# Performance work log

Measured on AMD Instinct MI355X. Metric: run time of the kernel, lower is better.

## Reference

```python
import jax, jax.numpy as jnp
import numpy as np

N_NODES = 100000
N_EDGES = 320000
DIM = 256


def _graph_conv(src, dst, h, W, b):
    # DGL GraphConv, norm='both', in_feats == out_feats (aggregate-then-transform)
    ones = jnp.ones((src.shape[0],), dtype=h.dtype)
    out_deg = jnp.clip(jax.ops.segment_sum(ones, src, num_segments=N_NODES), 1.0)
    in_deg = jnp.clip(jax.ops.segment_sum(ones, dst, num_segments=N_NODES), 1.0)
    h = h * (out_deg ** -0.5)[:, None]          # src-side normalization
    agg = jax.ops.segment_sum(h[src], dst, num_segments=N_NODES)  # SpMM (copy_u, sum)
    agg = agg * (in_deg ** -0.5)[:, None]       # dst-side normalization
    return agg @ W + b


def setup_inputs() -> dict:
    key = jax.random.key(0)
    ks = jax.random.split(key, 7)
    src = jax.random.randint(ks[0], (N_EDGES,), 0, N_NODES, dtype=jnp.int32)
    dst = jax.random.randint(ks[1], (N_EDGES,), 0, N_NODES, dtype=jnp.int32)
    node_feature = jax.random.normal(ks[2], (N_NODES, DIM), dtype=jnp.float32)
    s = 1.0 / np.sqrt(DIM)
    W1 = jax.random.normal(ks[3], (DIM, DIM), dtype=jnp.float32) * s
    b1 = jnp.zeros((DIM,), dtype=jnp.float32)
    W2 = jax.random.normal(ks[4], (DIM, DIM), dtype=jnp.float32) * s
    b2 = jnp.zeros((DIM,), dtype=jnp.float32)
    return {"src": src, "dst": dst, "node_feature": node_feature,
            "W1": W1, "b1": b1, "W2": W2, "b2": b2}


def reference(src, dst, node_feature, W1, b1, W2, b2):
    h = _graph_conv(src, dst, node_feature, W1, b1)
    h = _graph_conv(src, dst, jax.nn.relu(h), W2, b2)
    return jax.nn.relu(h)
```

## Files before the change

kernel.cpp:

```cpp
#include <hip/hip_runtime.h>

#define NN 100000
#define NE 320000
#define DIM 256
#define ELLW 32
#define FEAT_BLKS (NN * DIM / 4 / 256)

typedef _Float16 half8 __attribute__((ext_vector_type(8)));
typedef _Float16 half4v __attribute__((ext_vector_type(4)));
typedef float float4v __attribute__((ext_vector_type(4)));

__global__ void k_build(const int* __restrict__ src, const int* __restrict__ dst,
                        int* __restrict__ cnt_out, int* __restrict__ cnt_in,
                        int* __restrict__ ell) {
    int e = blockIdx.x * 256 + threadIdx.x;
    if (e < NE) {
        int s = src[e], d = dst[e];
        atomicAdd(&cnt_out[s], 1);
        int slot = atomicAdd(&cnt_in[d], 1);
        if (slot < ELLW) ell[d * ELLW + slot] = s * DIM;
    }
}

__global__ __launch_bounds__(256)
void k_prep(const float* __restrict__ feat, const int* __restrict__ cnt_out,
            _Float16* __restrict__ fh,
            const float* __restrict__ W1, const float* __restrict__ W2,
            _Float16* __restrict__ WT1, _Float16* __restrict__ WT2) {
    int b = blockIdx.x;
    if (b < FEAT_BLKS) {
        int i = b * 256 + threadIdx.x;
        int row = i >> 6;
        float w = rsqrtf(fmaxf((float)cnt_out[row], 1.f));
        float4 v = reinterpret_cast<const float4*>(feat)[i];
        half4v o;
        o[0] = (_Float16)(v.x * w); o[1] = (_Float16)(v.y * w);
        o[2] = (_Float16)(v.z * w); o[3] = (_Float16)(v.w * w);
        reinterpret_cast<half4v*>(fh)[i] = o;
    } else {
        int i = (b - FEAT_BLKS) * 256 + threadIdx.x;
        int k = i >> 8, n = i & 255;
        WT1[(size_t)n * DIM + k] = (_Float16)W1[(size_t)k * DIM + n];
        WT2[(size_t)n * DIM + k] = (_Float16)W2[(size_t)k * DIM + n];
    }
}

#define LDA 264

template <typename OutT, bool PRESCALE>
__global__ __launch_bounds__(512)
void k_fused(const int* __restrict__ deg, const int* __restrict__ ell,
             const _Float16* __restrict__ T,
             const _Float16* __restrict__ WT,
             const float* __restrict__ bias,
             const int* __restrict__ cnt_in, const int* __restrict__ cnt_out,
             OutT* __restrict__ out) {
    __shared__ _Float16 As[64 * LDA];

    const int t    = threadIdx.x;
    const int lane = t & 63;
    const int w    = t >> 6;
    const int bm   = blockIdx.x * 64;
    const int n0   = bm + w * 8;
    const int loff = lane << 2;

    int dgv  = min(deg[min(n0 + (lane & 7), NN - 1)], ELLW);
    int pre0 = ell[(size_t)min(n0 +     (lane >> 4), NN - 1) * ELLW + (lane & 15)];
    int pre1 = ell[(size_t)min(n0 + 4 + (lane >> 4), NN - 1) * ELLW + (lane & 15)];

    const half4v hz = {};
    float a0, a1, a2, a3;

#define ISSUE0(s, V0, V1, V2, V3, cap)                                         \
    {                                                                          \
        const int i_ = (s) >> 1;                                               \
        cap = (n0 + i_ < NN) ? __shfl(dgv, i_) : 0;                            \
        int pr_ = (i_ < 4) ? pre0 : pre1;                                      \
        int b_  = (i_ & 3) << 4;                                               \
        int s0_ = __shfl(pr_, b_ + 0), s1_ = __shfl(pr_, b_ + 1);              \
        int s2_ = __shfl(pr_, b_ + 2), s3_ = __shfl(pr_, b_ + 3);              \
        V0 = hz; V1 = hz; V2 = hz; V3 = hz;                                    \
        if (cap > 0) V0 = *reinterpret_cast<const half4v*>(T + (size_t)s0_ + loff); \
        if (cap > 1) V1 = *reinterpret_cast<const half4v*>(T + (size_t)s1_ + loff); \
        if (cap > 2) V2 = *reinterpret_cast<const half4v*>(T + (size_t)s2_ + loff); \
        if (cap > 3) V3 = *reinterpret_cast<const half4v*>(T + (size_t)s3_ + loff); \
    }

#define ISSUE1(s, V0, V1, V2, V3, cap)                                         \
    {                                                                          \
        const int i_ = (s) >> 1;                                               \
        if (cap > 4) {                                                         \
            int pr_ = (i_ < 4) ? pre0 : pre1;                                  \
            int b_  = (i_ & 3) << 4;                                           \
            int s0_ = __shfl(pr_, b_ + 4), s1_ = __shfl(pr_, b_ + 5);          \
            int s2_ = __shfl(pr_, b_ + 6), s3_ = __shfl(pr_, b_ + 7);          \
            V0 = hz; V1 = hz; V2 = hz; V3 = hz;                                \
            V0 = *reinterpret_cast<const half4v*>(T + (size_t)s0_ + loff);     \
            if (cap > 5) V1 = *reinterpret_cast<const half4v*>(T + (size_t)s1_ + loff); \
            if (cap > 6) V2 = *reinterpret_cast<const half4v*>(T + (size_t)s2_ + loff); \
            if (cap > 7) V3 = *reinterpret_cast<const half4v*>(T + (size_t)s3_ + loff); \
        }                                                                      \
    }

#define CONSUME0(s, V0, V1, V2, V3)                                            \
    {                                                                          \
        a0 = ((float)V0[0] + (float)V1[0]) + ((float)V2[0] + (float)V3[0]);    \
        a1 = ((float)V0[1] + (float)V1[1]) + ((float)V2[1] + (float)V3[1]);    \
        a2 = ((float)V0[2] + (float)V1[2]) + ((float)V2[2] + (float)V3[2]);    \
        a3 = ((float)V0[3] + (float)V1[3]) + ((float)V2[3] + (float)V3[3]);    \
    }

#define CONSUME1(s, V0, V1, V2, V3, cap)                                       \
    {                                                                          \
        const int i_ = (s) >> 1;                                               \
        if (cap > 4) {                                                         \
            a0 += ((float)V0[0] + (float)V1[0]) + ((float)V2[0] + (float)V3[0]); \
            a1 += ((float)V0[1] + (float)V1[1]) + ((float)V2[1] + (float)V3[1]); \
            a2 += ((float)V0[2] + (float)V1[2]) + ((float)V2[2] + (float)V3[2]); \
            a3 += ((float)V0[3] + (float)V1[3]) + ((float)V2[3] + (float)V3[3]); \
        }                                                                      \
        if (cap > 8) {                                   \
            int pr_ = (i_ < 4) ? pre0 : pre1;                                  \
            int b_  = (i_ & 3) << 4;                                           \
            for (int e = 8; e < cap && e < 16; ++e) {                          \
                int se = __shfl(pr_, b_ + e);                                  \
                half4v v = *reinterpret_cast<const half4v*>(T + (size_t)se + loff); \
                a0 += (float)v[0]; a1 += (float)v[1];                          \
                a2 += (float)v[2]; a3 += (float)v[3];                          \
            }                                                                  \
            for (int e = 16; e < cap; ++e) {      \
                int se = ell[(size_t)(n0 + i_) * ELLW + e];                    \
                half4v v = *reinterpret_cast<const half4v*>(T + (size_t)se + loff); \
                a0 += (float)v[0]; a1 += (float)v[1];                          \
                a2 += (float)v[2]; a3 += (float)v[3];                          \
            }                                                                  \
        }                                                                      \
        half4v o;                                                              \
        o[0] = (_Float16)a0; o[1] = (_Float16)a1;                              \
        o[2] = (_Float16)a2; o[3] = (_Float16)a3;                              \
        *reinterpret_cast<half4v*>(&As[(w * 8 + i_) * LDA + loff]) = o;        \
    }

    half4v A0, A1, A2, A3, B0, B1, B2, B3, C0, C1, C2, C3, D0, D1, D2, D3;
    int cA, cB, cC, cD;

    ISSUE0(0, A0, A1, A2, A3, cA)
    ISSUE1(1, B0, B1, B2, B3, cA)
    ISSUE0(2, C0, C1, C2, C3, cC)
    ISSUE1(3, D0, D1, D2, D3, cC)
    CONSUME0(0, A0, A1, A2, A3)               ISSUE0(4, A0, A1, A2, A3, cB)
    CONSUME1(1, B0, B1, B2, B3, cA)           ISSUE1(5, B0, B1, B2, B3, cB)
    CONSUME0(2, C0, C1, C2, C3)               ISSUE0(6, C0, C1, C2, C3, cD)
    CONSUME1(3, D0, D1, D2, D3, cC)           ISSUE1(7, D0, D1, D2, D3, cD)
    CONSUME0(4, A0, A1, A2, A3)               ISSUE0(8, A0, A1, A2, A3, cA)
    CONSUME1(5, B0, B1, B2, B3, cB)           ISSUE1(9, B0, B1, B2, B3, cA)
    CONSUME0(6, C0, C1, C2, C3)               ISSUE0(10, C0, C1, C2, C3, cC)
    CONSUME1(7, D0, D1, D2, D3, cD)           ISSUE1(11, D0, D1, D2, D3, cC)
    CONSUME0(8, A0, A1, A2, A3)               ISSUE0(12, A0, A1, A2, A3, cB)
    CONSUME1(9, B0, B1, B2, B3, cA)           ISSUE1(13, B0, B1, B2, B3, cB)
    CONSUME0(10, C0, C1, C2, C3)              ISSUE0(14, C0, C1, C2, C3, cD)
    CONSUME1(11, D0, D1, D2, D3, cC)          ISSUE1(15, D0, D1, D2, D3, cD)
    CONSUME0(12, A0, A1, A2, A3)
    CONSUME1(13, B0, B1, B2, B3, cB)
    CONSUME0(14, C0, C1, C2, C3)
    CONSUME1(15, D0, D1, D2, D3, cD)
#undef ISSUE0
#undef ISSUE1
#undef CONSUME0
#undef CONSUME1

    __syncthreads();

    const int l15 = lane & 15, quad = lane >> 4;
    const int colb = w * 32;
    const _Float16* bp0 = WT + (size_t)(colb +      l15) * DIM + quad * 8;
    const _Float16* bp1 = WT + (size_t)(colb + 16 + l15) * DIM + quad * 8;

    float4v acc4[4][2] = {};
    #pragma unroll
    for (int k0 = 0; k0 < DIM; k0 += 32) {
        half8 bf0 = *reinterpret_cast<const half8*>(bp0 + k0);
        half8 bf1 = *reinterpret_cast<const half8*>(bp1 + k0);
        half8 af[4];
        #pragma unroll
        for (int mt = 0; mt < 4; ++mt)
            af[mt] = *reinterpret_cast<half8*>(&As[(mt * 16 + l15) * LDA + quad * 8 + k0]);
        #pragma unroll
        for (int mt = 0; mt < 4; ++mt) {
            acc4[mt][0] = __builtin_amdgcn_mfma_f32_16x16x32_f16(af[mt], bf0, acc4[mt][0], 0, 0, 0);
            acc4[mt][1] = __builtin_amdgcn_mfma_f32_16x16x32_f16(af[mt], bf1, acc4[mt][1], 0, 0, 0);
        }
    }

    float bc0 = bias[colb + l15];
    float bc1 = bias[colb + 16 + l15];

    #pragma unroll
    for (int mt = 0; mt < 4; ++mt) {
        #pragma unroll
        for (int r = 0; r < 4; ++r) {
            int row = bm + mt * 16 + quad * 4 + r;
            if (row < NN) {
                float s  = rsqrtf(fmaxf((float)cnt_in[row], 1.f));
                float ps = PRESCALE ? rsqrtf(fmaxf((float)cnt_out[row], 1.f)) : 1.0f;
                float v0 = fmaxf(acc4[mt][0][r] * s + bc0, 0.f) * ps;
                float v1 = fmaxf(acc4[mt][1][r] * s + bc1, 0.f) * ps;
                out[(size_t)row * DIM + colb +      l15] = (OutT)v0;
                out[(size_t)row * DIM + colb + 16 + l15] = (OutT)v1;
            }
        }
    }
}

extern "C" void kernel_launch(void* const* d_in, const int* in_sizes, int n_in,
                              void* d_out, int out_size, void* d_ws, size_t ws_size,
                              hipStream_t stream) {
    const int*   src  = (const int*)d_in[0];
    const int*   dst  = (const int*)d_in[1];
    const float* feat = (const float*)d_in[2];
    const float* W1   = (const float*)d_in[3];
    const float* b1   = (const float*)d_in[4];
    const float* W2   = (const float*)d_in[5];
    const float* b2   = (const float*)d_in[6];
    float* out = (float*)d_out;

    int*      cnt_out = (int*)d_ws;
    int*      cnt_in  = cnt_out + NN;
    int*      ell     = cnt_in + NN;
    _Float16* WT1     = (_Float16*)(ell + (size_t)NN * ELLW);
    _Float16* WT2     = WT1 + DIM * DIM;
    _Float16* fh      = WT2 + DIM * DIM;
    _Float16* h1      = fh + (size_t)NN * DIM;

    hipMemsetAsync(d_ws, 0, (size_t)2 * NN * sizeof(int), stream);

    k_build<<<(NE + 255) / 256, 256, 0, stream>>>(src, dst, cnt_out, cnt_in, ell);
    k_prep <<<FEAT_BLKS + 256, 256, 0, stream>>>(feat, cnt_out, fh, W1, W2, WT1, WT2);

    const int ggrid = (NN + 63) / 64;

    k_fused<_Float16, true ><<<ggrid, 512, 0, stream>>>(cnt_in, ell, fh, WT1, b1, cnt_in, cnt_out, h1);
    k_fused<float,    false><<<ggrid, 512, 0, stream>>>(cnt_in, ell, h1, WT2, b2, cnt_in, cnt_out, out);
}
```

Measured before the change: 363.9 us.

## Convert fused aggregate-GEMM kernels to persistent blocks with atomic tile cursor

Both fused aggregation+GEMM kernels now launch a fixed grid of up to 1024 persistent 512-thread blocks. Each block repeatedly claims 64-row tiles through an atomic counter in workspace, which is zeroed by the existing memset. The aim is to cut block launch and scheduling overhead across about 1563 tiles and to balance the uneven per-tile gather cost dynamically. In exchange each tile now costs an atomic and two block barriers, and the per-tile prologue no longer overlaps across freshly launched blocks.

```diff
diff --git a/kernel.cpp b/kernel.cpp
--- a/kernel.cpp
+++ b/kernel.cpp
@@ -4,7 +4,9 @@
 #define NE 320000
 #define DIM 256
 #define ELLW 32
+#define NT ((NN + 63) / 64)
 #define FEAT_BLKS (NN * DIM / 4 / 256)
+#define PERSIST 1024
 
 typedef _Float16 half8 __attribute__((ext_vector_type(8)));
 typedef _Float16 half4v __attribute__((ext_vector_type(4)));
@@ -48,19 +50,18 @@
 #define LDA 264
 
 template <typename OutT, bool PRESCALE>
-__global__ __launch_bounds__(512)
-void k_fused(const int* __restrict__ deg, const int* __restrict__ ell,
-             const _Float16* __restrict__ T,
-             const _Float16* __restrict__ WT,
-             const float* __restrict__ bias,
-             const int* __restrict__ cnt_in, const int* __restrict__ cnt_out,
-             OutT* __restrict__ out) {
-    __shared__ _Float16 As[64 * LDA];
-
+__device__ __forceinline__
+void fused_tile(int tile, _Float16* As,
+                const int* __restrict__ deg, const int* __restrict__ ell,
+                const _Float16* __restrict__ T, const _Float16* __restrict__ WT,
+                const float* __restrict__ bias,
+                const int* __restrict__ cnt_in, const int* __restrict__ cnt_out,
+                OutT* __restrict__ out)
+{
     const int t    = threadIdx.x;
     const int lane = t & 63;
     const int w    = t >> 6;
-    const int bm   = blockIdx.x * 64;
+    const int bm   = tile * 64;
     const int n0   = bm + w * 8;
     const int loff = lane << 2;
 
@@ -212,6 +213,28 @@
     }
 }
 
+template <typename OutT, bool PRESCALE>
+__global__ __launch_bounds__(512)
+void k_fused(int* __restrict__ cursor,
+             const int* __restrict__ deg, const int* __restrict__ ell,
+             const _Float16* __restrict__ T, const _Float16* __restrict__ WT,
+             const float* __restrict__ bias,
+             const int* __restrict__ cnt_in, const int* __restrict__ cnt_out,
+             OutT* __restrict__ out) {
+    __shared__ _Float16 As[64 * LDA];
+    __shared__ int s_tile;
+
+    for (;;) {
+        __syncthreads();
+        if (threadIdx.x == 0) s_tile = atomicAdd(cursor, 1);
+        __syncthreads();
+        const int tile = s_tile;
+        if (tile >= NT) break;
+        fused_tile<OutT, PRESCALE>(tile, As, deg, ell, T, WT, bias,
+                                   cnt_in, cnt_out, out);
+    }
+}
+
 extern "C" void kernel_launch(void* const* d_in, const int* in_sizes, int n_in,
                               void* d_out, int out_size, void* d_ws, size_t ws_size,
                               hipStream_t stream) {
@@ -226,19 +249,20 @@
 
     int*      cnt_out = (int*)d_ws;
     int*      cnt_in  = cnt_out + NN;
-    int*      ell     = cnt_in + NN;
+    int*      cur     = cnt_in + NN;
+    int*      ell     = cur + 8;
     _Float16* WT1     = (_Float16*)(ell + (size_t)NN * ELLW);
     _Float16* WT2     = WT1 + DIM * DIM;
     _Float16* fh      = WT2 + DIM * DIM;
     _Float16* h1      = fh + (size_t)NN * DIM;
 
-    hipMemsetAsync(d_ws, 0, (size_t)2 * NN * sizeof(int), stream);
+    hipMemsetAsync(d_ws, 0, ((size_t)2 * NN + 8) * sizeof(int), stream);
 
     k_build<<<(NE + 255) / 256, 256, 0, stream>>>(src, dst, cnt_out, cnt_in, ell);
     k_prep <<<FEAT_BLKS + 256, 256, 0, stream>>>(feat, cnt_out, fh, W1, W2, WT1, WT2);
 
-    const int ggrid = (NN + 63) / 64;
-
-    k_fused<_Float16, true ><<<ggrid, 512, 0, stream>>>(cnt_in, ell, fh, WT1, b1, cnt_in, cnt_out, h1);
-    k_fused<float,    false><<<ggrid, 512, 0, stream>>>(cnt_in, ell, h1, WT2, b2, cnt_in, cnt_out, out);
-}
+    const int pgrid = (PERSIST < NT) ? PERSIST : NT;
+
+    k_fused<_Float16, true ><<<pgrid, 512, 0, stream>>>(cur + 0, cnt_in, ell, fh, WT1, b1, cnt_in, cnt_out, h1);
+    k_fused<float,    false><<<pgrid, 512, 0, stream>>>(cur + 1, cnt_in, ell, h1, WT2, b2, cnt_in, cnt_out, out);
+}
```

Measured after the change: 373.9 us. +2.7%, slower.

## Process two node tiles per block and prefetch second tile's metadata

Applied to the files above, without the earlier changes.

The fused gather+GEMM kernel now launches half as many blocks, and each block handles two 64-node tiles one after the other. The second tile's degree and ELL index loads are issued before the first tile's GEMM, so their latency can hide behind MFMA work. The aim is to cut block launch and scheduling overhead and to overlap metadata fetch with compute. In exchange, parallelism is halved (782 blocks of 512 threads), which may reduce latency hiding in the memory-bound gather phase, and there are extra syncthreads calls.

```diff
diff --git a/kernel.cpp b/kernel.cpp
--- a/kernel.cpp
+++ b/kernel.cpp
@@ -4,6 +4,8 @@
 #define NE 320000
 #define DIM 256
 #define ELLW 32
+#define NT ((NN + 63) / 64)
+#define GRID_F 782
 #define FEAT_BLKS (NN * DIM / 4 / 256)
 
 typedef _Float16 half8 __attribute__((ext_vector_type(8)));
@@ -47,26 +49,23 @@
 
 #define LDA 264
 
-template <typename OutT, bool PRESCALE>
-__global__ __launch_bounds__(512)
-void k_fused(const int* __restrict__ deg, const int* __restrict__ ell,
-             const _Float16* __restrict__ T,
-             const _Float16* __restrict__ WT,
-             const float* __restrict__ bias,
-             const int* __restrict__ cnt_in, const int* __restrict__ cnt_out,
-             OutT* __restrict__ out) {
-    __shared__ _Float16 As[64 * LDA];
-
-    const int t    = threadIdx.x;
-    const int lane = t & 63;
-    const int w    = t >> 6;
-    const int bm   = blockIdx.x * 64;
-    const int n0   = bm + w * 8;
+__device__ __forceinline__
+void load_meta(int tile, const int* __restrict__ deg, const int* __restrict__ ell,
+               int& dgv, int& pre0, int& pre1) {
+    const int lane = threadIdx.x & 63;
+    const int n0   = tile * 64 + (threadIdx.x >> 6) * 8;
+    dgv  = min(deg[min(n0 + (lane & 7), NN - 1)], ELLW);
+    pre0 = ell[(size_t)min(n0 +     (lane >> 4), NN - 1) * ELLW + (lane & 15)];
+    pre1 = ell[(size_t)min(n0 + 4 + (lane >> 4), NN - 1) * ELLW + (lane & 15)];
+}
+
+__device__ __forceinline__
+void gather_As(int tile, _Float16* As, int dgv, int pre0, int pre1,
+               const int* __restrict__ ell, const _Float16* __restrict__ T) {
+    const int lane = threadIdx.x & 63;
+    const int w    = threadIdx.x >> 6;
+    const int n0   = tile * 64 + w * 8;
     const int loff = lane << 2;
-
-    int dgv  = min(deg[min(n0 + (lane & 7), NN - 1)], ELLW);
-    int pre0 = ell[(size_t)min(n0 +     (lane >> 4), NN - 1) * ELLW + (lane & 15)];
-    int pre1 = ell[(size_t)min(n0 + 4 + (lane >> 4), NN - 1) * ELLW + (lane & 15)];
 
     const half4v hz = {};
     float a0, a1, a2, a3;
@@ -168,9 +167,17 @@
 #undef ISSUE1
 #undef CONSUME0
 #undef CONSUME1
-
-    __syncthreads();
-
+}
+
+template <typename OutT, bool PRESCALE>
+__device__ __forceinline__
+void gemm_As(int tile, const _Float16* As, const _Float16* __restrict__ WT,
+             const float* __restrict__ bias,
+             const int* __restrict__ cnt_in, const int* __restrict__ cnt_out,
+             OutT* __restrict__ out) {
+    const int lane = threadIdx.x & 63;
+    const int w    = threadIdx.x >> 6;
+    const int bm   = tile * 64;
     const int l15 = lane & 15, quad = lane >> 4;
     const int colb = w * 32;
     const _Float16* bp0 = WT + (size_t)(colb +      l15) * DIM + quad * 8;
@@ -184,7 +191,7 @@
         half8 af[4];
         #pragma unroll
         for (int mt = 0; mt < 4; ++mt)
-            af[mt] = *reinterpret_cast<half8*>(&As[(mt * 16 + l15) * LDA + quad * 8 + k0]);
+            af[mt] = *reinterpret_cast<const half8*>(&As[(mt * 16 + l15) * LDA + quad * 8 + k0]);
         #pragma unroll
         for (int mt = 0; mt < 4; ++mt) {
             acc4[mt][0] = __builtin_amdgcn_mfma_f32_16x16x32_f16(af[mt], bf0, acc4[mt][0], 0, 0, 0);
@@ -212,6 +219,36 @@
     }
 }
 
+template <typename OutT, bool PRESCALE>
+__global__ __launch_bounds__(512)
+void k_fused(const int* __restrict__ deg, const int* __restrict__ ell,
+             const _Float16* __restrict__ T, const _Float16* __restrict__ WT,
+             const float* __restrict__ bias,
+             const int* __restrict__ cnt_in, const int* __restrict__ cnt_out,
+             OutT* __restrict__ out) {
+    __shared__ _Float16 As[64 * LDA];
+
+    const int tileA = blockIdx.x;
+    const int tileB = blockIdx.x + GRID_F;
+
+    int dA, p0A, p1A;
+    load_meta(tileA, deg, ell, dA, p0A, p1A);
+    gather_As(tileA, As, dA, p0A, p1A, ell, T);
+
+    int dB = 0, p0B = 0, p1B = 0;
+    if (tileB < NT) load_meta(tileB, deg, ell, dB, p0B, p1B);
+
+    __syncthreads();
+    gemm_As<OutT, PRESCALE>(tileA, As, WT, bias, cnt_in, cnt_out, out);
+
+    if (tileB < NT) {
+        __syncthreads();
+        gather_As(tileB, As, dB, p0B, p1B, ell, T);
+        __syncthreads();
+        gemm_As<OutT, PRESCALE>(tileB, As, WT, bias, cnt_in, cnt_out, out);
+    }
+}
+
 extern "C" void kernel_launch(void* const* d_in, const int* in_sizes, int n_in,
                               void* d_out, int out_size, void* d_ws, size_t ws_size,
                               hipStream_t stream) {
@@ -237,8 +274,6 @@
     k_build<<<(NE + 255) / 256, 256, 0, stream>>>(src, dst, cnt_out, cnt_in, ell);
     k_prep <<<FEAT_BLKS + 256, 256, 0, stream>>>(feat, cnt_out, fh, W1, W2, WT1, WT2);
 
-    const int ggrid = (NN + 63) / 64;
-
-    k_fused<_Float16, true ><<<ggrid, 512, 0, stream>>>(cnt_in, ell, fh, WT1, b1, cnt_in, cnt_out, h1);
-    k_fused<float,    false><<<ggrid, 512, 0, stream>>>(cnt_in, ell, h1, WT2, b2, cnt_in, cnt_out, out);
-}
+    k_fused<_Float16, true ><<<GRID_F, 512, 0, stream>>>(cnt_in, ell, fh, WT1, b1, cnt_in, cnt_out, h1);
+    k_fused<float,    false><<<GRID_F, 512, 0, stream>>>(cnt_in, ell, h1, WT2, b2, cnt_in, cnt_out, out);
+}
```

Measured after the change: 378.1 us. +3.9%, slower.
